# Kernel tuning notes

Measured on AMD Instinct MI355X. Metric: run time of the kernel, lower is better.

## Reference

```python
import jax, jax.numpy as jnp
import numpy as np

N = 20000      # nodes
E = 320000     # directed edges (avg degree 16)
H = 4          # GAT attention heads
IN, HID, OUT = 5, 64, 32
DIMS = [(HID, HID), (HID, HID), (HID, OUT)]  # per-layer (in, out_per_head)


def setup_inputs() -> dict:
    keys = iter(jax.random.split(jax.random.key(0), 64))

    def rn(shape, s=0.1):
        return jax.random.normal(next(keys), shape, jnp.float32) * s

    inp = {
        "x": jax.random.normal(next(keys), (N, IN), jnp.float32),
        "edge_index": jax.random.randint(next(keys), (2, E), 0, N, dtype=jnp.int32),
        "enc_W": rn((IN, HID)), "enc_b": rn((HID,)),
    }
    for l, (din, dout) in enumerate(DIMS):
        inp["W%d" % l] = rn((din, H * dout))
        inp["as%d" % l] = rn((H, dout))
        inp["ad%d" % l] = rn((H, dout))
        inp["b%d" % l] = rn((dout,))
        inp["g%d" % l] = 1.0 + rn((dout,))
        inp["be%d" % l] = rn((dout,))
        inp["m%d" % l] = rn((dout,))
        inp["v%d" % l] = 1.0 + 0.1 * jax.random.uniform(next(keys), (dout,), jnp.float32)
    for h in ("eth", "man"):
        inp[h + "_W1"] = rn((OUT, OUT // 2)); inp[h + "_b1"] = rn((OUT // 2,))
        inp[h + "_W2"] = rn((OUT // 2, 1)); inp[h + "_b2"] = rn((1,))
    return inp


def _gat(x, src, dst, W, a_s, a_d, bias, n):
    # PyG GATConv: heads=H, concat=False (head mean), leaky_relu slope 0.2
    xp = (x @ W).reshape(n, H, -1)                        # [N,H,C]
    al_s = (xp * a_s).sum(-1)                             # [N,H]
    al_d = (xp * a_d).sum(-1)                             # [N,H]
    e = jax.nn.leaky_relu(al_s[src] + al_d[dst], 0.2)     # [E',H]
    emax = jax.ops.segment_max(e, dst, num_segments=n)    # stable softmax over in-edges
    ee = jnp.exp(e - emax[dst])
    den = jax.ops.segment_sum(ee, dst, num_segments=n)
    alpha = ee / (den[dst] + 1e-16)                       # [E',H]
    out = jax.ops.segment_sum(alpha[:, :, None] * xp[src], dst, num_segments=n)
    return out.mean(axis=1) + bias                        # [N,C]


def _bn(x, g, b, m, v):
    # BatchNorm1d, eval mode with running stats
    return (x - m) / jnp.sqrt(v + 1e-5) * g + b


def _head(z, W1, b1, W2, b2):
    # Linear -> ReLU -> (dropout off) -> Linear -> Sigmoid
    return jax.nn.sigmoid(jax.nn.relu(z @ W1 + b1) @ W2 + b2)


def _forward(x, src, dst, enc_W, enc_b, Ws, ASs, ADs, Bs, Gs, BEs, Ms, Vs, eth, man):
    n = x.shape[0]
    h = x @ enc_W + enc_b
    for l in range(3):
        h = _gat(h, src, dst, Ws[l], ASs[l], ADs[l], Bs[l], n)
        h = _bn(h, Gs[l], BEs[l], Ms[l], Vs[l])
        if l < 2:
            h = jax.nn.relu(h)
    graph_emb = h.mean(axis=0, keepdims=True)             # no `batch` attr branch
    ethics = _head(graph_emb, *eth)
    manip = _head(graph_emb, *man)
    return h, graph_emb, ethics, manip


def reference(x, edge_index, enc_W, enc_b,
              W0, as0, ad0, b0, g0, be0, m0, v0,
              W1, as1, ad1, b1, g1, be1, m1, v1,
              W2, as2, ad2, b2, g2, be2, m2, v2,
              eth_W1, eth_b1, eth_W2, eth_b2,
              man_W1, man_b1, man_W2, man_b2):
    n = x.shape[0]
    loops = jnp.arange(n, dtype=edge_index.dtype)
    src = jnp.concatenate([edge_index[0], loops])         # GATConv adds self-loops
    dst = jnp.concatenate([edge_index[1], loops])
    return _forward(x, src, dst, enc_W, enc_b,
                    [W0, W1, W2], [as0, as1, as2], [ad0, ad1, ad2], [b0, b1, b2],
                    [g0, g1, g2], [be0, be1, be2], [m0, m1, m2], [v0, v1, v2],
                    (eth_W1, eth_b1, eth_W2, eth_b2),
                    (man_W1, man_b1, man_W2, man_b2))
```

## Files before the change

kernel.cpp:

```cpp
#include <hip/hip_runtime.h>
#include <math.h>


#define H4 4

static __device__ __forceinline__ unsigned short f2bf(float f) {
  unsigned u = __float_as_uint(f);
  u += 0x7fffu + ((u >> 16) & 1u);
  return (unsigned short)(u >> 16);
}

__global__ void k_count(const int* __restrict__ dst, int* __restrict__ deg, int E) {
  int gid = blockIdx.x * blockDim.x + threadIdx.x;
  if (gid < E) atomicAdd(&deg[dst[gid]], 1);
}

__global__ void k_alloc(int* __restrict__ cursor, int* __restrict__ rbeg,
                        int* __restrict__ rend, int2* __restrict__ cs,
                        int* __restrict__ counter, int N) {
  int gid = blockIdx.x * blockDim.x + threadIdx.x;
  int lane = threadIdx.x & 63;
  int size = (gid < N) ? (cursor[gid] + 1) : 0;
  int v = size;
#pragma unroll
  for (int off = 1; off < 64; off <<= 1) {
    int t = __shfl_up(v, off, 64);
    if (lane >= off) v += t;
  }
  int tot = __shfl(v, 63, 64);
  int base = 0;
  if (lane == 63) base = atomicAdd(counter, tot);
  base = __shfl(base, 63, 64);
  if (gid < N) {
    int p = base + v - size;
    rbeg[gid] = p;
    rend[gid] = p + size;
    cs[p] = make_int2(gid, gid);
    cursor[gid] = p + 1;
  }
}

__global__ void k_scatter(const int* __restrict__ src, const int* __restrict__ dst,
                          int* __restrict__ cursor, int2* __restrict__ cs, int E) {
  int gid = blockIdx.x * blockDim.x + threadIdx.x;
  if (gid < E) {
    int d = dst[gid];
    int p = atomicAdd(&cursor[d], 1);
    cs[p] = make_int2(src[gid], d);
  }
}

template <int HC, bool ENC>
__global__ void k_gemm_al(const float* __restrict__ hin,
                          const float* __restrict__ encW, const float* __restrict__ encb,
                          const float* __restrict__ W,
                          const float* __restrict__ a_s, const float* __restrict__ a_d,
                          unsigned short* __restrict__ xpb,
                          float* __restrict__ als, float* __restrict__ ald, int N) {
  constexpr int K = 64, NB = 16, C = HC / H4;
  __shared__ float hs[NB * K];
  int n0 = blockIdx.x * NB;
  int tid = threadIdx.x;
  if (ENC) {
    for (int idx = tid; idx < NB * K; idx += HC) {
      int i = idx >> 6, j = idx & 63;
      int n = n0 + i;
      float a = 0.f;
      if (n < N) {
        a = encb[j];
#pragma unroll
        for (int k = 0; k < 5; ++k) a += hin[n * 5 + k] * encW[k * 64 + j];
      }
      hs[idx] = a;
    }
  } else {
    for (int idx = tid; idx < NB * K; idx += HC) {
      int n = n0 + (idx >> 6);
      hs[idx] = (n < N) ? hin[(size_t)n0 * K + idx] : 0.f;
    }
  }
  __syncthreads();
  float acc[NB];
#pragma unroll
  for (int i = 0; i < NB; ++i) acc[i] = 0.f;
  for (int k = 0; k < K; k += 4) {
    float w0 = W[(k + 0) * HC + tid];
    float w1 = W[(k + 1) * HC + tid];
    float w2 = W[(k + 2) * HC + tid];
    float w3 = W[(k + 3) * HC + tid];
#pragma unroll
    for (int i = 0; i < NB; ++i) {
      float4 hv = *(const float4*)&hs[i * K + k];
      acc[i] += hv.x * w0 + hv.y * w1 + hv.z * w2 + hv.w * w3;
    }
  }
#pragma unroll
  for (int i = 0; i < NB; ++i) {
    int n = n0 + i;
    if (n < N) xpb[(size_t)n * HC + tid] = f2bf(acc[i]);
  }
  float as_w = a_s[tid], ad_w = a_d[tid];
  int c = tid & (C - 1);
  int h = tid / C;
#pragma unroll
  for (int i = 0; i < NB; ++i) {
    float vs = acc[i] * as_w, vd = acc[i] * ad_w;
#pragma unroll
    for (int off = C >> 1; off; off >>= 1) {
      vs += __shfl_xor(vs, off, 64);
      vd += __shfl_xor(vd, off, 64);
    }
    int n = n0 + i;
    if (c == 0 && n < N) {
      als[n * H4 + h] = vs;
      ald[n * H4 + h] = vd;
    }
  }
}

__global__ void k_ee(const int2* __restrict__ cs, const float* __restrict__ als,
                     const float* __restrict__ ald, float* __restrict__ ee, int M) {
  int gid = blockIdx.x * blockDim.x + threadIdx.x;
  if (gid >= M * H4) return;
  int j = gid >> 2, h = gid & 3;
  int2 sd = cs[j];
  float e = als[sd.x * H4 + h] + ald[sd.y * H4 + h];
  e = (e > 0.f) ? e : 0.2f * e;
  ee[gid] = __expf(e);
}

template <int C, bool RELU>
__global__ void k_gather(const unsigned short* __restrict__ xpb, const float* __restrict__ ee,
                         const int* __restrict__ rbeg, const int* __restrict__ rend,
                         const int2* __restrict__ cs,
                         const float* __restrict__ bias, const float* __restrict__ g,
                         const float* __restrict__ be, const float* __restrict__ m,
                         const float* __restrict__ v, float* __restrict__ hout, int N) {
  constexpr int HC = H4 * C;
  constexpr int VPL = HC / 64;
  int wave = threadIdx.x >> 6;
  int lane = threadIdx.x & 63;
  int n = blockIdx.x * 2 + wave;
  if (n >= N) return;
  int h = lane >> 4;
  int beg = rbeg[n], end = rend[n];

  float s = 0.f;
  float acc[VPL];
#pragma unroll
  for (int i = 0; i < VPL; ++i) acc[i] = 0.f;

  int j = beg;
  for (; j + 1 < end; j += 2) {
    int s0 = cs[j].x, s1 = cs[j + 1].x;
    float e0 = ee[j * H4 + h], e1 = ee[j * H4 + H4 + h];
    s += e0 + e1;
    if constexpr (VPL == 4) {
      uint2 u0 = *(const uint2*)(xpb + (size_t)s0 * HC + lane * 4);
      uint2 u1 = *(const uint2*)(xpb + (size_t)s1 * HC + lane * 4);
      acc[0] += e0 * __uint_as_float(u0.x << 16) + e1 * __uint_as_float(u1.x << 16);
      acc[1] += e0 * __uint_as_float(u0.x & 0xffff0000u) + e1 * __uint_as_float(u1.x & 0xffff0000u);
      acc[2] += e0 * __uint_as_float(u0.y << 16) + e1 * __uint_as_float(u1.y << 16);
      acc[3] += e0 * __uint_as_float(u0.y & 0xffff0000u) + e1 * __uint_as_float(u1.y & 0xffff0000u);
    } else {
      unsigned u0 = *(const unsigned*)(xpb + (size_t)s0 * HC + lane * 2);
      unsigned u1 = *(const unsigned*)(xpb + (size_t)s1 * HC + lane * 2);
      acc[0] += e0 * __uint_as_float(u0 << 16) + e1 * __uint_as_float(u1 << 16);
      acc[1] += e0 * __uint_as_float(u0 & 0xffff0000u) + e1 * __uint_as_float(u1 & 0xffff0000u);
    }
  }
  if (j < end) {
    int s0 = cs[j].x;
    float e0 = ee[j * H4 + h];
    s += e0;
    if constexpr (VPL == 4) {
      uint2 u0 = *(const uint2*)(xpb + (size_t)s0 * HC + lane * 4);
      acc[0] += e0 * __uint_as_float(u0.x << 16);
      acc[1] += e0 * __uint_as_float(u0.x & 0xffff0000u);
      acc[2] += e0 * __uint_as_float(u0.y << 16);
      acc[3] += e0 * __uint_as_float(u0.y & 0xffff0000u);
    } else {
      unsigned u0 = *(const unsigned*)(xpb + (size_t)s0 * HC + lane * 2);
      acc[0] += e0 * __uint_as_float(u0 << 16);
      acc[1] += e0 * __uint_as_float(u0 & 0xffff0000u);
    }
  }

  float inv = 1.f / (s + 1e-16f);
#pragma unroll
  for (int i = 0; i < VPL; ++i) {
    acc[i] *= inv;
    acc[i] += __shfl_xor(acc[i], 16, 64);
    acc[i] += __shfl_xor(acc[i], 32, 64);
  }

  if (lane < 16) {
    int c0 = lane * VPL;
    float o[VPL];
#pragma unroll
    for (int i = 0; i < VPL; ++i) {
      int cc = c0 + i;
      float t = acc[i] * (1.f / H4) + bias[cc];
      t = (t - m[cc]) * rsqrtf(v[cc] + 1e-5f) * g[cc] + be[cc];
      if (RELU) t = fmaxf(t, 0.f);
      o[i] = t;
    }
    if constexpr (VPL == 4)
      *(float4*)&hout[(size_t)n * C + c0] = make_float4(o[0], o[1], o[2], o[3]);
    else
      *(float2*)&hout[(size_t)n * C + c0] = make_float2(o[0], o[1]);
  }
}

__global__ void k_reduce(const float* __restrict__ hfin, float* __restrict__ gacc, int N) {
  __shared__ float lds[256];
  int tid = threadIdx.x;
  int c = tid & 31;
  int rowStart = blockIdx.x * (blockDim.x / 32) + (tid >> 5);
  int rowStride = gridDim.x * (blockDim.x / 32);
  float acc = 0.f;
  for (int n = rowStart; n < N; n += rowStride) acc += hfin[(size_t)n * 32 + c];
  lds[tid] = acc;
  __syncthreads();
  if (tid < 32) {
    float s = 0.f;
#pragma unroll
    for (int i = 0; i < 8; ++i) s += lds[i * 32 + tid];
    atomicAdd(&gacc[tid], s);
  }
}

__global__ void k_heads(const float* __restrict__ gacc,
                        const float* __restrict__ eW1, const float* __restrict__ eb1,
                        const float* __restrict__ eW2, const float* __restrict__ eb2,
                        const float* __restrict__ mW1, const float* __restrict__ mb1,
                        const float* __restrict__ mW2, const float* __restrict__ mb2,
                        float* __restrict__ out, int N) {
  __shared__ float z[32];
  __shared__ float hid[32];
  int tid = threadIdx.x;
  size_t base = (size_t)N * 32;
  if (tid < 32) {
    float zv = gacc[tid] / (float)N;
    z[tid] = zv;
    out[base + tid] = zv;
  }
  __syncthreads();
  if (tid < 16) {
    float a = eb1[tid], b = mb1[tid];
    for (int k = 0; k < 32; ++k) {
      a += z[k] * eW1[k * 16 + tid];
      b += z[k] * mW1[k * 16 + tid];
    }
    hid[tid] = fmaxf(a, 0.f);
    hid[16 + tid] = fmaxf(b, 0.f);
  }
  __syncthreads();
  if (tid == 0) {
    float a = eb2[0];
    for (int k = 0; k < 16; ++k) a += hid[k] * eW2[k];
    out[base + 32] = 1.f / (1.f + __expf(-a));
  } else if (tid == 1) {
    float a = mb2[0];
    for (int k = 0; k < 16; ++k) a += hid[16 + k] * mW2[k];
    out[base + 33] = 1.f / (1.f + __expf(-a));
  }
}

extern "C" void kernel_launch(void* const* d_in, const int* in_sizes, int n_in,
                              void* d_out, int out_size, void* d_ws, size_t ws_size,
                              hipStream_t stream) {
  const int N = in_sizes[0] / 5;
  const int E = in_sizes[1] / 2;
  const int M = E + N;

  const float* x = (const float*)d_in[0];
  const int* ei = (const int*)d_in[1];
  const int* e_src = ei;
  const int* e_dst = ei + E;
  const float* encW = (const float*)d_in[2];
  const float* encb = (const float*)d_in[3];
  const float* Wl[3]; const float* asl[3]; const float* adl[3]; const float* bl[3];
  const float* gl[3]; const float* bel[3]; const float* ml[3]; const float* vl[3];
  for (int l = 0; l < 3; ++l) {
    const int o = 4 + 8 * l;
    Wl[l]  = (const float*)d_in[o + 0];
    asl[l] = (const float*)d_in[o + 1];
    adl[l] = (const float*)d_in[o + 2];
    bl[l]  = (const float*)d_in[o + 3];
    gl[l]  = (const float*)d_in[o + 4];
    bel[l] = (const float*)d_in[o + 5];
    ml[l]  = (const float*)d_in[o + 6];
    vl[l]  = (const float*)d_in[o + 7];
  }
  const float* eW1 = (const float*)d_in[28];
  const float* eb1 = (const float*)d_in[29];
  const float* eW2 = (const float*)d_in[30];
  const float* eb2 = (const float*)d_in[31];
  const float* mW1 = (const float*)d_in[32];
  const float* mb1 = (const float*)d_in[33];
  const float* mW2 = (const float*)d_in[34];
  const float* mb2 = (const float*)d_in[35];

  float* out = (float*)d_out;

  float* wf = (float*)d_ws;
  size_t off = 0;
  float* hA   = wf + off; off += (size_t)N * 64;
  float* hB   = wf + off; off += (size_t)N * 64;
  unsigned short* xpb = (unsigned short*)(wf + off); off += (size_t)N * 128;
  float* als  = wf + off; off += (size_t)N * 4;
  float* ald  = wf + off; off += (size_t)N * 4;
  float* ee   = wf + off; off += (size_t)M * 4;
  float* gacc = wf + off; off += 32;
  int* wi = (int*)(wf + off);
  int2* cs     = (int2*)wi;
  int* rbeg    = wi + 2 * M;
  int* rend    = rbeg + N;
  int* cursor  = rend + N;
  int* counter = cursor + N;

  const int T = 256;
  const int gN  = (N + T - 1) / T;
  const int gE  = (E + T - 1) / T;
  const int gEE = (M * 4 + T - 1) / T;
  const int gGE = (N + 15) / 16;
  const int gGA = (N + 1) / 2;

  hipMemsetAsync(cursor, 0, (size_t)(N + 1) * sizeof(int), stream);
  hipMemsetAsync(gacc, 0, 32 * sizeof(float), stream);
  k_count<<<gE, T, 0, stream>>>(e_dst, cursor, E);
  k_alloc<<<gN, T, 0, stream>>>(cursor, rbeg, rend, cs, counter, N);
  k_scatter<<<gE, T, 0, stream>>>(e_src, e_dst, cursor, cs, E);

  k_gemm_al<256, true><<<gGE, 256, 0, stream>>>(x, encW, encb, Wl[0], asl[0], adl[0],
                                                xpb, als, ald, N);
  k_ee<<<gEE, T, 0, stream>>>(cs, als, ald, ee, M);
  k_gather<64, true><<<gGA, 128, 0, stream>>>(xpb, ee, rbeg, rend, cs,
                                              bl[0], gl[0], bel[0], ml[0], vl[0], hB, N);

  k_gemm_al<256, false><<<gGE, 256, 0, stream>>>(hB, encW, encb, Wl[1], asl[1], adl[1],
                                                 xpb, als, ald, N);
  k_ee<<<gEE, T, 0, stream>>>(cs, als, ald, ee, M);
  k_gather<64, true><<<gGA, 128, 0, stream>>>(xpb, ee, rbeg, rend, cs,
                                              bl[1], gl[1], bel[1], ml[1], vl[1], hA, N);

  k_gemm_al<128, false><<<gGE, 128, 0, stream>>>(hA, encW, encb, Wl[2], asl[2], adl[2],
                                                 xpb, als, ald, N);
  k_ee<<<gEE, T, 0, stream>>>(cs, als, ald, ee, M);
  k_gather<32, false><<<gGA, 128, 0, stream>>>(xpb, ee, rbeg, rend, cs,
                                               bl[2], gl[2], bel[2], ml[2], vl[2], out, N);

  k_reduce<<<80, 256, 0, stream>>>(out, gacc, N);
  k_heads<<<1, 64, 0, stream>>>(gacc, eW1, eb1, eW2, eb2, mW1, mb1, mW2, mb2, out, N);
}
```

Baseline: 371.3 us.

## Fuse edge attention exp into gather kernel and shrink CSR to int col

Removes the separate per-edge exp kernel and its ee buffer. The gather kernel now reads als[src] and computes leaky_relu and exp on the fly, using a per-node ald value loaded once. The CSR array stores only the source index instead of (src,dst) pairs, which halves index traffic. The gacc memset is folded into k_alloc. The change trades three launches plus the ee write/read for redundant exp work in the gather, since each of the 16 lanes in a head recomputes it, and adds an extra dependent als gather.

Measured after the change: 355.8 us. 1.04x faster.

```diff
diff --git a/kernel.cpp b/kernel.cpp
--- a/kernel.cpp
+++ b/kernel.cpp
@@ -16,10 +16,11 @@
 }
 
 __global__ void k_alloc(int* __restrict__ cursor, int* __restrict__ rbeg,
-                        int* __restrict__ rend, int2* __restrict__ cs,
-                        int* __restrict__ counter, int N) {
+                        int* __restrict__ rend, int* __restrict__ col,
+                        int* __restrict__ counter, float* __restrict__ gacc, int N) {
   int gid = blockIdx.x * blockDim.x + threadIdx.x;
   int lane = threadIdx.x & 63;
+  if (gid < 32) gacc[gid] = 0.f;
   int size = (gid < N) ? (cursor[gid] + 1) : 0;
   int v = size;
 #pragma unroll
@@ -35,18 +36,17 @@
     int p = base + v - size;
     rbeg[gid] = p;
     rend[gid] = p + size;
-    cs[p] = make_int2(gid, gid);
+    col[p] = gid;
     cursor[gid] = p + 1;
   }
 }
 
 __global__ void k_scatter(const int* __restrict__ src, const int* __restrict__ dst,
-                          int* __restrict__ cursor, int2* __restrict__ cs, int E) {
+                          int* __restrict__ cursor, int* __restrict__ col, int E) {
   int gid = blockIdx.x * blockDim.x + threadIdx.x;
   if (gid < E) {
-    int d = dst[gid];
-    int p = atomicAdd(&cursor[d], 1);
-    cs[p] = make_int2(src[gid], d);
+    int p = atomicAdd(&cursor[dst[gid]], 1);
+    col[p] = src[gid];
   }
 }
 
@@ -118,21 +118,11 @@
   }
 }
 
-__global__ void k_ee(const int2* __restrict__ cs, const float* __restrict__ als,
-                     const float* __restrict__ ald, float* __restrict__ ee, int M) {
-  int gid = blockIdx.x * blockDim.x + threadIdx.x;
-  if (gid >= M * H4) return;
-  int j = gid >> 2, h = gid & 3;
-  int2 sd = cs[j];
-  float e = als[sd.x * H4 + h] + ald[sd.y * H4 + h];
-  e = (e > 0.f) ? e : 0.2f * e;
-  ee[gid] = __expf(e);
-}
-
 template <int C, bool RELU>
-__global__ void k_gather(const unsigned short* __restrict__ xpb, const float* __restrict__ ee,
+__global__ void k_gather(const unsigned short* __restrict__ xpb,
+                         const float* __restrict__ als, const float* __restrict__ ald,
                          const int* __restrict__ rbeg, const int* __restrict__ rend,
-                         const int2* __restrict__ cs,
+                         const int* __restrict__ col,
                          const float* __restrict__ bias, const float* __restrict__ g,
                          const float* __restrict__ be, const float* __restrict__ m,
                          const float* __restrict__ v, float* __restrict__ hout, int N) {
@@ -143,6 +133,7 @@
   int n = blockIdx.x * 2 + wave;
   if (n >= N) return;
   int h = lane >> 4;
+  float aldn = ald[n * H4 + h];
   int beg = rbeg[n], end = rend[n];
 
   float s = 0.f;
@@ -152,8 +143,10 @@
 
   int j = beg;
   for (; j + 1 < end; j += 2) {
-    int s0 = cs[j].x, s1 = cs[j + 1].x;
-    float e0 = ee[j * H4 + h], e1 = ee[j * H4 + H4 + h];
+    int s0 = col[j], s1 = col[j + 1];
+    float a0 = als[s0 * H4 + h], a1 = als[s1 * H4 + h];
+    float e0 = a0 + aldn; e0 = (e0 > 0.f) ? e0 : 0.2f * e0; e0 = __expf(e0);
+    float e1 = a1 + aldn; e1 = (e1 > 0.f) ? e1 : 0.2f * e1; e1 = __expf(e1);
     s += e0 + e1;
     if constexpr (VPL == 4) {
       uint2 u0 = *(const uint2*)(xpb + (size_t)s0 * HC + lane * 4);
@@ -170,8 +163,9 @@
     }
   }
   if (j < end) {
-    int s0 = cs[j].x;
-    float e0 = ee[j * H4 + h];
+    int s0 = col[j];
+    float a0 = als[s0 * H4 + h];
+    float e0 = a0 + aldn; e0 = (e0 > 0.f) ? e0 : 0.2f * e0; e0 = __expf(e0);
     s += e0;
     if constexpr (VPL == 4) {
       uint2 u0 = *(const uint2*)(xpb + (size_t)s0 * HC + lane * 4);
@@ -311,11 +305,10 @@
   unsigned short* xpb = (unsigned short*)(wf + off); off += (size_t)N * 128;
   float* als  = wf + off; off += (size_t)N * 4;
   float* ald  = wf + off; off += (size_t)N * 4;
-  float* ee   = wf + off; off += (size_t)M * 4;
   float* gacc = wf + off; off += 32;
   int* wi = (int*)(wf + off);
-  int2* cs     = (int2*)wi;
-  int* rbeg    = wi + 2 * M;
+  int* col     = wi;
+  int* rbeg    = col + M;
   int* rend    = rbeg + N;
   int* cursor  = rend + N;
   int* counter = cursor + N;
@@ -323,32 +316,27 @@
   const int T = 256;
   const int gN  = (N + T - 1) / T;
   const int gE  = (E + T - 1) / T;
-  const int gEE = (M * 4 + T - 1) / T;
   const int gGE = (N + 15) / 16;
   const int gGA = (N + 1) / 2;
 
   hipMemsetAsync(cursor, 0, (size_t)(N + 1) * sizeof(int), stream);
-  hipMemsetAsync(gacc, 0, 32 * sizeof(float), stream);
   k_count<<<gE, T, 0, stream>>>(e_dst, cursor, E);
-  k_alloc<<<gN, T, 0, stream>>>(cursor, rbeg, rend, cs, counter, N);
-  k_scatter<<<gE, T, 0, stream>>>(e_src, e_dst, cursor, cs, E);
+  k_alloc<<<gN, T, 0, stream>>>(cursor, rbeg, rend, col, counter, gacc, N);
+  k_scatter<<<gE, T, 0, stream>>>(e_src, e_dst, cursor, col, E);
 
   k_gemm_al<256, true><<<gGE, 256, 0, stream>>>(x, encW, encb, Wl[0], asl[0], adl[0],
                                                 xpb, als, ald, N);
-  k_ee<<<gEE, T, 0, stream>>>(cs, als, ald, ee, M);
-  k_gather<64, true><<<gGA, 128, 0, stream>>>(xpb, ee, rbeg, rend, cs,
+  k_gather<64, true><<<gGA, 128, 0, stream>>>(xpb, als, ald, rbeg, rend, col,
                                               bl[0], gl[0], bel[0], ml[0], vl[0], hB, N);
 
   k_gemm_al<256, false><<<gGE, 256, 0, stream>>>(hB, encW, encb, Wl[1], asl[1], adl[1],
                                                  xpb, als, ald, N);
-  k_ee<<<gEE, T, 0, stream>>>(cs, als, ald, ee, M);
-  k_gather<64, true><<<gGA, 128, 0, stream>>>(xpb, ee, rbeg, rend, cs,
+  k_gather<64, true><<<gGA, 128, 0, stream>>>(xpb, als, ald, rbeg, rend, col,
                                               bl[1], gl[1], bel[1], ml[1], vl[1], hA, N);
 
   k_gemm_al<128, false><<<gGE, 128, 0, stream>>>(hA, encW, encb, Wl[2], asl[2], adl[2],
                                                  xpb, als, ald, N);
-  k_ee<<<gEE, T, 0, stream>>>(cs, als, ald, ee, M);
-  k_gather<32, false><<<gGA, 128, 0, stream>>>(xpb, ee, rbeg, rend, cs,
+  k_gather<32, false><<<gGA, 128, 0, stream>>>(xpb, als, ald, rbeg, rend, col,
                                                bl[2], gl[2], bel[2], ml[2], vl[2], out, N);
 
   k_reduce<<<80, 256, 0, stream>>>(out, gacc, N);
```
